# Kernel tuning notes

Hardware: AMD Instinct MI355X
Metric: run time of the kernel (lower is better)

The kernel has to match this reference:

```python
import jax, jax.numpy as jnp
import numpy as np

B, S, T, H, E, V = 64, 512, 12, 256, 256, 50000


def _xavier(key, shape):
    lim = np.sqrt(6.0 / (shape[0] + shape[1]))
    return jax.random.uniform(key, shape, jnp.float32, -lim, lim)


def setup_inputs() -> dict:
    key = jax.random.key(0)
    ks = jax.random.split(key, 14)
    return {
        "input_ids": jax.random.randint(ks[0], (B, S), 0, V),
        "tree_ids": jax.random.randint(ks[1], (B, T, S), 0, S),
        "tree_ids_r": jax.random.randint(ks[2], (B, T, S), 0, S),
        "tree_ids_l": jax.random.randint(ks[3], (B, T, S), 0, S),
        "emb": _xavier(ks[4], (V, E)),
        "W_ioux": _xavier(ks[5], (E, 3 * H)),
        "b_ioux": jnp.zeros((3 * H,), jnp.float32),
        "U_iou_r": _xavier(ks[6], (H, 3 * H)),
        "U_iou_l": _xavier(ks[7], (H, 3 * H)),
        "W_f": _xavier(ks[8], (E, H)),
        "b_f": jnp.zeros((H,), jnp.float32),
        "U_f0": _xavier(ks[9], (H, H)),
        "U_f1": _xavier(ks[10], (H, H)),
        "U_f2": _xavier(ks[11], (H, H)),
        "U_f3": _xavier(ks[12], (H, H)),
    }


def reference(input_ids, tree_ids, tree_ids_r, tree_ids_l, emb,
              W_ioux, b_ioux, U_iou_r, U_iou_l, W_f, b_f,
              U_f0, U_f1, U_f2, U_f3):
    x = emb[input_ids]                      # [B, S, E]
    Bn, Sn = x.shape[0], x.shape[1]
    Hn = U_f0.shape[0]
    bidx = jnp.arange(Bn)[:, None]          # [B, 1] batch index for scatter

    def take(a, idx):                       # gather along node dim: out[b,s]=a[b,idx[b,s]]
        return jnp.take_along_axis(a, idx[..., None], axis=1)

    iou_x = x @ W_ioux + b_ioux             # precompute; constant across steps
    f_x = x @ W_f + b_f

    def step(carry, ids):
        h, c = carry
        td, tr, tl = ids                    # each [B, S]
        # which parent nodes receive children this step (node 0 excluded)
        counts = jnp.zeros((Bn, Sn), x.dtype).at[bidx, td].add(1.0)
        mask = (counts.at[:, 0].set(0.0) > 0)[..., None]  # [B, S, 1]
        # scatter-add child hidden projections into parent iou preactivations
        iou = iou_x.at[bidx, tr].add(h @ U_iou_r)
        iou = iou.at[bidx, tl].add(h @ U_iou_l)
        i, o, u = jnp.split(iou, 3, axis=-1)
        i, o, u = jax.nn.sigmoid(i), jax.nn.sigmoid(o), jnp.tanh(u)
        # forget gate per child: gather parent fx and child-hidden projections
        f = jax.nn.sigmoid(take(f_x, td)
                           + take(h @ U_f0 + h @ U_f1, tr)
                           + take(h @ U_f2 + h @ U_f3, tl))
        c_new = (i * u).at[bidx, td].add(f * c)
        h_new = o * jnp.tanh(c_new)
        h = jnp.where(mask, h_new, h)
        c = jnp.where(mask, c_new, c)
        return (h, c), None

    h0 = jnp.zeros((Bn, Sn, Hn), x.dtype)
    ids = (jnp.swapaxes(tree_ids, 0, 1),
           jnp.swapaxes(tree_ids_r, 0, 1),
           jnp.swapaxes(tree_ids_l, 0, 1))   # [T, B, S]
    (h, c), _ = jax.lax.scan(step, (h0, h0), ids)

    roots = tree_ids[:, -1, :].max(axis=1)   # [B]
    h_root = h[jnp.arange(Bn), roots]        # [B, H]
    return h, c, h_root
```

## Files before the change

kernel.cpp:

```cpp
#include <hip/hip_runtime.h>
#include <stdint.h>

#define B_ 64
#define S_ 512
#define T_ 12
#define M_ (B_*S_)
#define NP_ 2048

typedef __attribute__((ext_vector_type(8))) short bf16x8;
typedef __attribute__((ext_vector_type(4))) float f32x4;

__device__ __forceinline__ uint16_t f2bf(float f){
  union { float f; uint32_t u; } x; x.f = f;
  uint32_t r = x.u + 0x7FFFu + ((x.u >> 16) & 1u);
  return (uint16_t)(r >> 16);
}
__device__ __forceinline__ float bf2f(uint16_t u){
  union { float f; uint32_t u; } x; x.u = ((uint32_t)u) << 16; return x.f;
}
__device__ __forceinline__ float sigm(float x){ return 1.0f/(1.0f + expf(-x)); }
__device__ __forceinline__ float4 bf4(const uint16_t* p){
  const ushort4 v = *reinterpret_cast<const ushort4*>(p);
  return make_float4(bf2f(v.x), bf2f(v.y), bf2f(v.z), bf2f(v.w));
}

__device__ __forceinline__ void gload16(const uint16_t* g, uint16_t* l){
  __builtin_amdgcn_global_load_lds(
      (const __attribute__((address_space(1))) uint32_t*)g,
      (__attribute__((address_space(3))) uint32_t*)l, 16, 0, 0);
}

__global__ void zero16(uint4* __restrict__ p, long n16){
  const long i = (long)blockIdx.x * 256 + threadIdx.x;
  if (i < n16) p[i] = make_uint4(0,0,0,0);
}
__global__ void bf16_to_f32(const uint16_t* __restrict__ src, float* __restrict__ dst, long n){
  const long i = ((long)blockIdx.x * 256 + threadIdx.x) * 4;
  if (i + 3 < n) {
    const float4 o = bf4(src + i);
    *reinterpret_cast<float4*>(dst + i) = o;
  }
}

__global__ void build_ucatT(const float* __restrict__ Ur, const float* __restrict__ Ul,
                            const float* __restrict__ f0, const float* __restrict__ f1,
                            const float* __restrict__ f2, const float* __restrict__ f3,
                            uint16_t* __restrict__ UcatT){
  const int idx = blockIdx.x * 256 + threadIdx.x;
  const int n = idx >> 8, k = idx & 255;
  float v;
  if (n < 768)        v = Ur[k*768 + n];
  else if (n < 1536)  v = Ul[k*768 + (n-768)];
  else if (n < 1792) { int j = n-1536; v = f0[k*256+j] + f1[k*256+j]; }
  else               { int j = n-1792; v = f2[k*256+j] + f3[k*256+j]; }
  UcatT[(long)n*256 + k] = f2bf(v);
}

__global__ void build_wallT(const float* __restrict__ Wioux, const float* __restrict__ Wf,
                            uint16_t* __restrict__ WT){
  const int idx = blockIdx.x * 256 + threadIdx.x;
  const int n = idx >> 8, k = idx & 255;
  const float v = (n < 768) ? Wioux[(long)k*768 + n] : Wf[(long)k*256 + (n-768)];
  WT[(long)n*256 + k] = f2bf(v);
}

__global__ void gather_embg(const float* __restrict__ emb, const int* __restrict__ ids,
                            uint16_t* __restrict__ out){
  const int wave = threadIdx.x >> 6, lane = threadIdx.x & 63;
  const long row = (long)blockIdx.x*4 + wave;
  const long rid = (long)ids[row];
  const float4 v = *reinterpret_cast<const float4*>(emb + rid*256 + lane*4);
  ushort4 o; o.x=f2bf(v.x); o.y=f2bf(v.y); o.z=f2bf(v.z); o.w=f2bf(v.w);
  *reinterpret_cast<ushort4*>(out + row*256 + lane*4) = o;
}

__global__ __launch_bounds__(256)
void gemm_pipe(const uint16_t* __restrict__ A, const uint16_t* __restrict__ BT,
               const float* __restrict__ bias, const float* __restrict__ bias2, int split,
               uint16_t* __restrict__ C, int N, int NT)
{
  __shared__ __align__(16) uint16_t As[2][4096];
  __shared__ __align__(16) uint16_t Bs[2][4096];
  const int tid = threadIdx.x, lane = tid & 63, wave = tid >> 6;
  const int wr = wave >> 1, wc = wave & 1;
  const int id = blockIdx.x, rx = id & 7, q = id >> 3;
  const int mt = rx + 8*(q / NT);
  const int nt = q % NT;
  const long m0 = (long)mt * 128;
  const int  n0 = nt * 128;

  const int rl0 = wave*32 + (lane >> 2);
  const int rl1 = rl0 + 16;
  const int sg0 = (lane & 3) ^ ((rl0 >> 1) & 3);
  const int sg1 = (lane & 3) ^ ((rl1 >> 1) & 3);
  const uint16_t* ga0 = A + (m0 + rl0)*256 + sg0*8;
  const uint16_t* ga1 = A + (m0 + rl1)*256 + sg1*8;
  const uint16_t* gb0 = BT + (long)(n0 + rl0)*256 + sg0*8;
  const uint16_t* gb1 = BT + (long)(n0 + rl1)*256 + sg1*8;

  f32x4 acc[4][4];
  #pragma unroll
  for (int i=0;i<4;i++)
    #pragma unroll
    for (int j=0;j<4;j++) acc[i][j] = (f32x4){0.f,0.f,0.f,0.f};

  const int l15 = lane & 15, lseg = lane >> 4;
  int aoff[4], boff[4];
  #pragma unroll
  for (int i=0;i<4;i++){ const int m = wr*64 + i*16 + l15; aoff[i] = m*32 + ((lseg ^ ((m>>1)&3))<<3); }
  #pragma unroll
  for (int j=0;j<4;j++){ const int n = wc*64 + j*16 + l15; boff[j] = n*32 + ((lseg ^ ((n>>1)&3))<<3); }

  {
    uint16_t* a = &As[0][wave*1024];
    uint16_t* b = &Bs[0][wave*1024];
    gload16(ga0, a); gload16(ga1, a + 512);
    gload16(gb0, b); gload16(gb1, b + 512);
  }
  asm volatile("s_waitcnt vmcnt(0)" ::: "memory");
  __builtin_amdgcn_s_barrier();

  #pragma unroll
  for (int tt = 0; tt < 8; ++tt) {
    if (tt < 7) {
      const int nb = (tt + 1) & 1;
      const int ks = (tt + 1) * 32;
      uint16_t* a = &As[nb][wave*1024];
      uint16_t* b = &Bs[nb][wave*1024];
      gload16(ga0 + ks, a); gload16(ga1 + ks, a + 512);
      gload16(gb0 + ks, b); gload16(gb1 + ks, b + 512);
    }
    const int cb = tt & 1;
    bf16x8 af[4], bfv[4];
    #pragma unroll
    for (int i=0;i<4;i++) af[i]  = *reinterpret_cast<const bf16x8*>(&As[cb][aoff[i]]);
    #pragma unroll
    for (int j=0;j<4;j++) bfv[j] = *reinterpret_cast<const bf16x8*>(&Bs[cb][boff[j]]);
    #pragma unroll
    for (int i=0;i<4;i++)
      #pragma unroll
      for (int j=0;j<4;j++)
        acc[i][j] = __builtin_amdgcn_mfma_f32_16x16x32_bf16(af[i], bfv[j], acc[i][j], 0, 0, 0);
    if (tt < 7) {
      asm volatile("s_waitcnt vmcnt(0)" ::: "memory");
      __builtin_amdgcn_s_barrier();
    }
  }

  const int rquad = lane >> 4;
  #pragma unroll
  for (int j=0;j<4;j++){
    const int col = n0 + wc*64 + j*16 + l15;
    const float bv = bias ? ((col < split) ? bias[col] : bias2[col - split]) : 0.0f;
    #pragma unroll
    for (int i=0;i<4;i++){
      const long rbase = m0 + wr*64 + i*16 + rquad*4;
      #pragma unroll
      for (int r=0;r<4;r++)
        C[(rbase + r)*N + col] = f2bf(acc[i][j][r] + bv);
    }
  }
}

__global__ void build_csr(const int* __restrict__ td_g, const int* __restrict__ tr_g,
                          const int* __restrict__ tl_g,
                          int* __restrict__ csr_off, int* __restrict__ csr_val){
  const int t = blockIdx.x >> 6;
  const int b = blockIdx.x & 63;
  __shared__ int ids[S_];
  __shared__ int cnt[S_];
  __shared__ int off[S_];
  __shared__ int chc[8][S_];
  const int s = threadIdx.x;
  const int q = s >> 6;
  const int* srcs[3] = {td_g, tr_g, tl_g};
  for (int arr = 0; arr < 3; ++arr) {
    const int myid = srcs[arr][((long)b*T_ + t)*S_ + s];
    ids[s] = myid;
    cnt[s] = 0;
    #pragma unroll
    for (int qq=0; qq<8; qq++) chc[qq][s] = 0;
    __syncthreads();
    atomicAdd(&cnt[myid], 1);
    atomicAdd(&chc[q][myid], 1);
    __syncthreads();
    int rank = 0;
    for (int qq = 0; qq < q; ++qq) rank += chc[qq][myid];
    for (int i = q*64; i < s; ++i) rank += (ids[i] == myid) ? 1 : 0;
    off[s] = cnt[s];
    __syncthreads();
    for (int w = 1; w < S_; w <<= 1){
      const int v = (s >= w) ? off[s-w] : 0;
      __syncthreads();
      off[s] += v;
      __syncthreads();
    }
    const long base = (((long)arr*T_ + t)*B_ + b);
    int* offs = csr_off + base*(S_+1);
    int* vals = csr_val + base*S_;
    offs[s] = off[s] - cnt[s];
    if (s == S_-1) offs[S_] = off[s];
    vals[(off[myid] - cnt[myid]) + rank] = s;
    __syncthreads();
  }
}

__global__ __launch_bounds__(256)
void t0_update(uint16_t* __restrict__ h, uint16_t* __restrict__ c_out,
               const uint16_t* __restrict__ ioufx, const int* __restrict__ csr_off)
{
  const int wave = threadIdx.x >> 6, lane = threadIdx.x & 63;
  const long bs = (long)blockIdx.x*4 + wave;
  const int b = (int)(bs >> 9), s = (int)(bs & 511);
  const int j = lane * 4;
  const int* off_td = csr_off + (long)b*(S_+1);
  if (s == 0 || off_td[s+1] <= off_td[s]) return;
  const long ib = bs*1024;
  const float4 ai = bf4(ioufx + ib + j);
  const float4 ao = bf4(ioufx + ib + 256 + j);
  const float4 au = bf4(ioufx + ib + 512 + j);
  float4 cacc;
  cacc.x = sigm(ai.x)*tanhf(au.x); cacc.y = sigm(ai.y)*tanhf(au.y);
  cacc.z = sigm(ai.z)*tanhf(au.z); cacc.w = sigm(ai.w)*tanhf(au.w);
  ushort4 ho, co;
  ho.x = f2bf(sigm(ao.x)*tanhf(cacc.x)); ho.y = f2bf(sigm(ao.y)*tanhf(cacc.y));
  ho.z = f2bf(sigm(ao.z)*tanhf(cacc.z)); ho.w = f2bf(sigm(ao.w)*tanhf(cacc.w));
  co.x = f2bf(cacc.x); co.y = f2bf(cacc.y); co.z = f2bf(cacc.z); co.w = f2bf(cacc.w);
  *reinterpret_cast<ushort4*>(h + bs*256 + j) = ho;
  *reinterpret_cast<ushort4*>(c_out + bs*256 + j) = co;
}

__global__ __launch_bounds__(256)
void step_update(uint16_t* __restrict__ h,
                 const uint16_t* __restrict__ c_in, uint16_t* __restrict__ c_out,
                 const uint16_t* __restrict__ P,
                 const uint16_t* __restrict__ ioufx,
                 const int* __restrict__ csr_off, const int* __restrict__ csr_val,
                 const int* __restrict__ tr_g, const int* __restrict__ tl_g,
                 int t, int row0)
{
  const int wave = threadIdx.x >> 6, lane = threadIdx.x & 63;
  const int id = blockIdx.x, rx = id & 7, q = id >> 3;
  const int b_local = rx + 8*(q >> 7);
  const int rg = q & 127;
  const long bs = (long)row0 + b_local*512 + rg*4 + wave;
  const int b = (int)(bs >> 9), s = (int)(bs & 511);
  const int j = lane * 4;

  const int* off_td = csr_off + (((long)0*T_ + t)*B_ + b)*(S_+1);
  const int td0 = off_td[s], td1 = off_td[s+1];
  const bool masked = (s != 0) && (td1 > td0);
  if (!masked) {
    *reinterpret_cast<ushort4*>(c_out + bs*256 + j) =
        *reinterpret_cast<const ushort4*>(c_in + bs*256 + j);
    return;
  }
  const int* off_tr = csr_off + (((long)1*T_ + t)*B_ + b)*(S_+1);
  const int* off_tl = csr_off + (((long)2*T_ + t)*B_ + b)*(S_+1);
  const int* val_td = csr_val + (((long)0*T_ + t)*B_ + b)*S_;
  const int* val_tr = csr_val + (((long)1*T_ + t)*B_ + b)*S_;
  const int* val_tl = csr_val + (((long)2*T_ + t)*B_ + b)*S_;

  const long lbase = (long)(b<<9) - row0;

  const long ib = bs*1024;
  float4 ai = bf4(ioufx + ib + j);
  float4 ao = bf4(ioufx + ib + 256 + j);
  float4 au = bf4(ioufx + ib + 512 + j);
  for (int p = off_tr[s]; p < off_tr[s+1]; ++p) {
    const long pr = (lbase + val_tr[p]) * NP_;
    const float4 x = bf4(P + pr + j), y = bf4(P + pr + 256 + j), z = bf4(P + pr + 512 + j);
    ai.x+=x.x; ai.y+=x.y; ai.z+=x.z; ai.w+=x.w;
    ao.x+=y.x; ao.y+=y.y; ao.z+=y.z; ao.w+=y.w;
    au.x+=z.x; au.y+=z.y; au.z+=z.z; au.w+=z.w;
  }
  for (int p = off_tl[s]; p < off_tl[s+1]; ++p) {
    const long pr = (lbase + val_tl[p]) * NP_;
    const float4 x = bf4(P + pr + 768 + j), y = bf4(P + pr + 1024 + j), z = bf4(P + pr + 1280 + j);
    ai.x+=x.x; ai.y+=x.y; ai.z+=x.z; ai.w+=x.w;
    ao.x+=y.x; ao.y+=y.y; ao.z+=y.z; ao.w+=y.w;
    au.x+=z.x; au.y+=z.y; au.z+=z.z; au.w+=z.w;
  }
  float4 cacc;
  cacc.x = sigm(ai.x)*tanhf(au.x); cacc.y = sigm(ai.y)*tanhf(au.y);
  cacc.z = sigm(ai.z)*tanhf(au.z); cacc.w = sigm(ai.w)*tanhf(au.w);
  const float4 fxv = bf4(ioufx + ib + 768 + j);
  const int* trrow = tr_g + ((long)b*T_ + t)*S_;
  const int* tlrow = tl_g + ((long)b*T_ + t)*S_;
  for (int p = td0; p < td1; ++p) {
    const int sp = val_td[p];
    const long prr = (lbase + trrow[sp]) * NP_ + 1536;
    const long prl = (lbase + tlrow[sp]) * NP_ + 1792;
    const float4 pa = bf4(P + prr + j), pb = bf4(P + prl + j);
    const float4 cv = bf4(c_in + ((long)(b<<9) + sp)*256 + j);
    cacc.x += sigm(fxv.x + pa.x + pb.x) * cv.x;
    cacc.y += sigm(fxv.y + pa.y + pb.y) * cv.y;
    cacc.z += sigm(fxv.z + pa.z + pb.z) * cv.z;
    cacc.w += sigm(fxv.w + pa.w + pb.w) * cv.w;
  }
  ushort4 ho, co;
  ho.x = f2bf(sigm(ao.x) * tanhf(cacc.x));
  ho.y = f2bf(sigm(ao.y) * tanhf(cacc.y));
  ho.z = f2bf(sigm(ao.z) * tanhf(cacc.z));
  ho.w = f2bf(sigm(ao.w) * tanhf(cacc.w));
  co.x = f2bf(cacc.x); co.y = f2bf(cacc.y); co.z = f2bf(cacc.z); co.w = f2bf(cacc.w);
  *reinterpret_cast<ushort4*>(h + bs*256 + j) = ho;
  *reinterpret_cast<ushort4*>(c_out + bs*256 + j) = co;
}

__global__ void root_kernel(const uint16_t* __restrict__ h, const int* __restrict__ td_g,
                            float* __restrict__ out_root){
  const int b = blockIdx.x;
  __shared__ int red[256];
  const int* td = td_g + ((long)b*T_ + (T_-1))*S_;
  int m = 0;
  for (int s = threadIdx.x; s < S_; s += 256) m = max(m, td[s]);
  red[threadIdx.x] = m; __syncthreads();
  for (int w = 128; w > 0; w >>= 1){
    if (threadIdx.x < w) red[threadIdx.x] = max(red[threadIdx.x], red[threadIdx.x+w]);
    __syncthreads();
  }
  const int root = red[0];
  out_root[b*256 + threadIdx.x] = bf2f(h[((long)b*512 + root)*256 + threadIdx.x]);
}

extern "C" void kernel_launch(void* const* d_in, const int* in_sizes, int n_in,
                              void* d_out, int out_size, void* d_ws, size_t ws_size,
                              hipStream_t stream) {
  const int*   input_ids  = (const int*)  d_in[0];
  const int*   tree_ids   = (const int*)  d_in[1];
  const int*   tree_ids_r = (const int*)  d_in[2];
  const int*   tree_ids_l = (const int*)  d_in[3];
  const float* emb        = (const float*)d_in[4];
  const float* W_ioux     = (const float*)d_in[5];
  const float* b_ioux     = (const float*)d_in[6];
  const float* W_f        = (const float*)d_in[9];
  const float* b_f        = (const float*)d_in[10];
  float* out = (float*)d_out;

  size_t woff = 0;
  auto alloc = [&](size_t bytes)->char*{
    char* p = (char*)d_ws + woff; woff += (bytes + 255) & ~(size_t)255; return p;
  };
  uint16_t* ioufx  = (uint16_t*)alloc((size_t)M_*1024*2);
  uint16_t* hA     = (uint16_t*)alloc((size_t)M_*256*2);
  uint16_t* cA     = (uint16_t*)alloc((size_t)M_*256*2);
  uint16_t* cB     = (uint16_t*)alloc((size_t)M_*256*2);
  int* csr_off     = (int*)     alloc((size_t)3*T_*B_*(S_+1)*4);
  int* csr_val     = (int*)     alloc((size_t)3*T_*B_*S_*4);
  uint16_t* UcatT  = (uint16_t*)alloc((size_t)NP_*256*2);
  uint16_t* WallT  = (uint16_t*)alloc((size_t)1024*256*2);
  int CB = 64;
  while (CB > 8 && woff + (size_t)CB*S_*NP_*2 > ws_size) CB >>= 1;
  uint16_t* P      = (uint16_t*)alloc((size_t)CB*S_*NP_*2);
  uint16_t* embg   = P;

  build_ucatT<<<2048, 256, 0, stream>>>((const float*)d_in[7], (const float*)d_in[8],
      (const float*)d_in[11], (const float*)d_in[12], (const float*)d_in[13], (const float*)d_in[14],
      UcatT);
  build_wallT<<<1024, 256, 0, stream>>>(W_ioux, W_f, WallT);
  gather_embg<<<M_/4, 256, 0, stream>>>(emb, input_ids, embg);
  gemm_pipe<<<(M_/128)*8, 256, 0, stream>>>(embg, WallT, b_ioux, b_f, 768, ioufx, 1024, 8);
  build_csr<<<T_*B_, S_, 0, stream>>>(tree_ids, tree_ids_r, tree_ids_l, csr_off, csr_val);
  zero16<<<12288, 256, 0, stream>>>((uint4*)hA, 3145728L);

  uint16_t *cc = cA, *cn = cB;
  t0_update<<<M_/4, 256, 0, stream>>>(hA, cn, ioufx, csr_off);
  { uint16_t* tc = cc; cc = cn; cn = tc; }
  for (int t = 1; t < T_; ++t) {
    for (int b0 = 0; b0 < B_; b0 += CB) {
      const int row0 = b0 * S_;
      const int Mc   = CB * S_;
      gemm_pipe<<<(Mc/128)*16, 256, 0, stream>>>(hA + (long)row0*256, UcatT,
                                                 nullptr, nullptr, 0, P, NP_, 16);
      step_update<<<CB*128, 256, 0, stream>>>(hA, cc, cn, P, ioufx,
                                              csr_off, csr_val, tree_ids_r, tree_ids_l,
                                              t, row0);
    }
    uint16_t* tc = cc; cc = cn; cn = tc;
  }

  bf16_to_f32<<<8192, 256, 0, stream>>>(hA, out, (long)M_*256);
  bf16_to_f32<<<8192, 256, 0, stream>>>(cc, out + (long)M_*256, (long)M_*256);
  root_kernel<<<B_, 256, 0, stream>>>(hA, tree_ids, out + 2L*M_*256);
}
```

Measured before the change: 1.179 ms.

## Triple-buffer GEMM loads and stage epilogue through LDS for coalesced stores

The bf16 GEMM moves from double to triple buffering of its A/B tiles. Loads are issued two tiles ahead, and a partial vmcnt wait lets the next tile's loads stay in flight while the current tile is consumed. The epilogue now writes the accumulators into a padded LDS tile in two halves, then writes them out with 16-byte coalesced stores instead of scattered 2-byte ones. This costs more shared memory, which may lower occupancy, and adds extra barriers in the epilogue.

```diff
diff --git a/kernel.cpp b/kernel.cpp
--- a/kernel.cpp
+++ b/kernel.cpp
@@ -79,8 +79,8 @@
                const float* __restrict__ bias, const float* __restrict__ bias2, int split,
                uint16_t* __restrict__ C, int N, int NT)
 {
-  __shared__ __align__(16) uint16_t As[2][4096];
-  __shared__ __align__(16) uint16_t Bs[2][4096];
+  __shared__ __align__(16) uint16_t As[3][4096];
+  __shared__ __align__(16) uint16_t Bs[3][4096];
   const int tid = threadIdx.x, lane = tid & 63, wave = tid >> 6;
   const int wr = wave >> 1, wc = wave & 1;
   const int id = blockIdx.x, rx = id & 7, q = id >> 3;
@@ -111,26 +111,24 @@
   #pragma unroll
   for (int j=0;j<4;j++){ const int n = wc*64 + j*16 + l15; boff[j] = n*32 + ((lseg ^ ((n>>1)&3))<<3); }
 
-  {
-    uint16_t* a = &As[0][wave*1024];
-    uint16_t* b = &Bs[0][wave*1024];
-    gload16(ga0, a); gload16(ga1, a + 512);
-    gload16(gb0, b); gload16(gb1, b + 512);
-  }
-  asm volatile("s_waitcnt vmcnt(0)" ::: "memory");
-  __builtin_amdgcn_s_barrier();
+  #define STAGE(tile, buf) {                                   \
+    const int ks_ = (tile)*32;                                 \
+    uint16_t* a_ = &As[(buf)][wave*1024];                      \
+    uint16_t* b_ = &Bs[(buf)][wave*1024];                      \
+    gload16(ga0 + ks_, a_); gload16(ga1 + ks_, a_ + 512);      \
+    gload16(gb0 + ks_, b_); gload16(gb1 + ks_, b_ + 512);      \
+  }
+
+  STAGE(0, 0)
+  STAGE(1, 1)
 
   #pragma unroll
   for (int tt = 0; tt < 8; ++tt) {
-    if (tt < 7) {
-      const int nb = (tt + 1) & 1;
-      const int ks = (tt + 1) * 32;
-      uint16_t* a = &As[nb][wave*1024];
-      uint16_t* b = &Bs[nb][wave*1024];
-      gload16(ga0 + ks, a); gload16(ga1 + ks, a + 512);
-      gload16(gb0 + ks, b); gload16(gb1 + ks, b + 512);
-    }
-    const int cb = tt & 1;
+    if (tt < 7) asm volatile("s_waitcnt vmcnt(4)" ::: "memory");
+    else        asm volatile("s_waitcnt vmcnt(0)" ::: "memory");
+    __builtin_amdgcn_s_barrier();
+    if (tt < 6) STAGE(tt + 2, (tt + 2) % 3)
+    const int cb = tt % 3;
     bf16x8 af[4], bfv[4];
     #pragma unroll
     for (int i=0;i<4;i++) af[i]  = *reinterpret_cast<const bf16x8*>(&As[cb][aoff[i]]);
@@ -141,24 +139,39 @@
       #pragma unroll
       for (int j=0;j<4;j++)
         acc[i][j] = __builtin_amdgcn_mfma_f32_16x16x32_bf16(af[i], bfv[j], acc[i][j], 0, 0, 0);
-    if (tt < 7) {
-      asm volatile("s_waitcnt vmcnt(0)" ::: "memory");
-      __builtin_amdgcn_s_barrier();
-    }
-  }
-
+  }
+  #undef STAGE
+
+  __syncthreads();
+  uint16_t* ep = &As[0][0];
   const int rquad = lane >> 4;
+  const int rowq = tid >> 4;
+  const int cseg = tid & 15;
+  float bv[4];
   #pragma unroll
   for (int j=0;j<4;j++){
     const int col = n0 + wc*64 + j*16 + l15;
-    const float bv = bias ? ((col < split) ? bias[col] : bias2[col - split]) : 0.0f;
-    #pragma unroll
-    for (int i=0;i<4;i++){
-      const long rbase = m0 + wr*64 + i*16 + rquad*4;
+    bv[j] = bias ? ((col < split) ? bias[col] : bias2[col - split]) : 0.0f;
+  }
+  #pragma unroll
+  for (int half = 0; half < 2; ++half) {
+    if (wr == half) {
       #pragma unroll
-      for (int r=0;r<4;r++)
-        C[(rbase + r)*N + col] = f2bf(acc[i][j][r] + bv);
+      for (int i=0;i<4;i++)
+        #pragma unroll
+        for (int j=0;j<4;j++)
+          #pragma unroll
+          for (int r=0;r<4;r++)
+            ep[(i*16 + rquad*4 + r)*136 + wc*64 + j*16 + l15] = f2bf(acc[i][j][r] + bv[j]);
     }
+    __syncthreads();
+    #pragma unroll
+    for (int it=0; it<4; ++it) {
+      const int r2 = it*16 + rowq;
+      const uint4 v = *reinterpret_cast<const uint4*>(&ep[r2*136 + cseg*8]);
+      *reinterpret_cast<uint4*>(C + (m0 + half*64 + r2)*N + n0 + cseg*8) = v;
+    }
+    __syncthreads();
   }
 }
 
```

Result: slower. 1.217 ms (+3.3%).
